# Kernel optimization log

Measured on AMD Instinct MI355X. Metric: run time of the kernel, lower is better.

## Reference

```python
import jax, jax.numpy as jnp
import numpy as np

GRAPH_SIZE = 128
ROWS = 3
COLS = 3
BATCH = 4096


def setup_inputs() -> dict:
    key = jax.random.key(0)
    k1, k2 = jax.random.split(key)
    x = jax.random.uniform(k1, (BATCH, GRAPH_SIZE, GRAPH_SIZE), dtype=jnp.float32)
    # kaiming_normal_ on a [rows, cols] 2D tensor: fan_in = cols, std = sqrt(2/fan_in)
    coef = jax.random.normal(k2, (ROWS, COLS), dtype=jnp.float32) * np.float32(np.sqrt(2.0 / COLS))
    return {"x": x, "coef": coef}


def reference(x, coef):
    # Faithful vectorized form of FACoef.forward.
    # Original per-sample math:
    #   a_series[0] = x@x ; a_series[i+1] = x @ a_series[i]   (a_series[i] = x^(i+2))
    #   term[i, j] = trace(ones @ a_series[i])**(j+1) / numel(x)**(i+j+2)
    # and trace(ones @ A) == sum of all entries of A.
    rows, cols = coef.shape
    G = x.shape[-1]
    x = x.reshape(-1, G, G)  # [B, G, G]
    n = jnp.float32(G * G)   # numel per graph

    p0 = jnp.matmul(x, x)    # x^2, [B, G, G]

    def step(p, _):
        s = p.sum(axis=(1, 2))          # trace(1 @ p) == sum(p), [B]
        return jnp.matmul(x, p), s      # next power x^(k+1)

    _, s = jax.lax.scan(step, p0, None, length=rows)  # s: [rows, B], s[i] = sum(x^(i+2))

    i = jnp.arange(rows, dtype=jnp.float32)[:, None, None]  # [rows,1,1]
    j = jnp.arange(cols, dtype=jnp.float32)[None, None, :]  # [1,1,cols]
    # terms: [rows, B, cols]
    terms = s[:, :, None] ** (j + 1.0) / n ** (i + j + 2.0)
    # per-sample scalar: sum(coef * terms.view(rows, cols))
    return jnp.sum(coef[:, None, :] * terms, axis=(0, 2))  # [B]
```

## Files before the change

kernel.cpp:

```cpp
#include <hip/hip_runtime.h>


#define G 128

typedef float v4f __attribute__((ext_vector_type(4)));

__global__ __launch_bounds__(512, 4) void facoef_kernel(
    const float* __restrict__ x, const float* __restrict__ coef,
    float* __restrict__ out) {
  const int b = blockIdx.x;
  const int tid = threadIdx.x;
  const int cg = tid & 31;
  const int rh = tid >> 5;

  __shared__ float part[16][128];
  __shared__ float u[128];
  __shared__ float Sp[3][2];

  const float* xb = x + (size_t)b * (G * G);

  v4f xs[8];
#pragma unroll
  for (int r = 0; r < 8; ++r) {
    xs[r] = *(const v4f*)(xb + (rh * 8 + r) * G + cg * 4);
  }

  v4f acc = xs[0];
#pragma unroll
  for (int r = 1; r < 8; ++r) acc += xs[r];
  *(v4f*)&part[rh][cg * 4] = acc;
  __syncthreads();

  if (tid < 128) {
    float s = 0.f;
#pragma unroll
    for (int h = 0; h < 16; ++h) s += part[h][tid];
    u[tid] = s;
  }
  __syncthreads();

  for (int k = 0; k < 3; ++k) {
    v4f a = {0.f, 0.f, 0.f, 0.f};
#pragma unroll
    for (int r = 0; r < 8; ++r) {
      float uv = u[rh * 8 + r];
      a += uv * xs[r];
    }
    *(v4f*)&part[rh][cg * 4] = a;
    __syncthreads();

    if (tid < 128) {
      float s = 0.f;
#pragma unroll
      for (int h = 0; h < 16; ++h) s += part[h][tid];
      float t = s;
#pragma unroll
      for (int off = 32; off > 0; off >>= 1) t += __shfl_xor(t, off, 64);
      if ((tid & 63) == 0) Sp[k][tid >> 6] = t;
      if (k < 2) u[tid] = s;
    }
    __syncthreads();
  }

  if (tid == 0) {
    double S[3];
#pragma unroll
    for (int k = 0; k < 3; ++k) S[k] = (double)Sp[k][0] + (double)Sp[k][1];
    const double n = (double)(G * G);
    double np[7];
    np[2] = n * n;
    np[3] = np[2] * n;
    np[4] = np[3] * n;
    np[5] = np[4] * n;
    np[6] = np[5] * n;
    double o = 0.0;
#pragma unroll
    for (int i = 0; i < 3; ++i) {
      double s1 = S[i], s2 = s1 * s1, s3 = s2 * s1;
      double sp[3] = {s1, s2, s3};
#pragma unroll
      for (int j = 0; j < 3; ++j) {
        o += (double)coef[i * 3 + j] * sp[j] / np[i + j + 2];
      }
    }
    out[b] = (float)o;
  }
}

extern "C" void kernel_launch(void* const* d_in, const int* in_sizes, int n_in,
                              void* d_out, int out_size, void* d_ws, size_t ws_size,
                              hipStream_t stream) {
  const float* x = (const float*)d_in[0];
  const float* coef = (const float*)d_in[1];
  float* out = (float*)d_out;
  const int batch = in_sizes[0] / (G * G);
  facoef_kernel<<<batch, 512, 0, stream>>>(x, coef, out);
}
```

Baseline: 45.79 us.

## Compute power sums via left/right vector products to cut sequential passes

Instead of three sequential passes of u<-u^T x, the kernel computes the column-sum vector u1 and the row-sum vector v1 = x·1 in the first pass. It then forms u2 = u1^T x and v2 = x v1 in one pass and gets sum(x^2), sum(x^3) and sum(x^4) as dot products u1·v1, u2·v1 and u2·v2. This removes one full pass over the register tile and several block barriers, at the cost of extra shuffle reductions. The occupancy hint is also raised to 8 blocks per CU.

New measurement: 47.36 us. 3.4% more time.

```diff
diff --git a/kernel.cpp b/kernel.cpp
--- a/kernel.cpp
+++ b/kernel.cpp
@@ -5,62 +5,95 @@
 
 typedef float v4f __attribute__((ext_vector_type(4)));
 
-__global__ __launch_bounds__(512, 4) void facoef_kernel(
+__global__ __launch_bounds__(512, 8) void facoef_kernel(
     const float* __restrict__ x, const float* __restrict__ coef,
     float* __restrict__ out) {
   const int b = blockIdx.x;
   const int tid = threadIdx.x;
   const int cg = tid & 31;
   const int rh = tid >> 5;
+  const int lane = tid & 63;
 
   __shared__ float part[16][128];
-  __shared__ float u[128];
+  __shared__ float u1s[128], v1s[128], v2s[128];
   __shared__ float Sp[3][2];
 
   const float* xb = x + (size_t)b * (G * G);
 
   v4f xs[8];
 #pragma unroll
-  for (int r = 0; r < 8; ++r) {
+  for (int r = 0; r < 8; ++r)
     xs[r] = *(const v4f*)(xb + (rh * 8 + r) * G + cg * 4);
-  }
 
   v4f acc = xs[0];
 #pragma unroll
   for (int r = 1; r < 8; ++r) acc += xs[r];
   *(v4f*)&part[rh][cg * 4] = acc;
+
+  float rs[8];
+#pragma unroll
+  for (int r = 0; r < 8; ++r) rs[r] = xs[r].x + xs[r].y + xs[r].z + xs[r].w;
+#pragma unroll
+  for (int off = 1; off < 32; off <<= 1) {
+#pragma unroll
+    for (int r = 0; r < 8; ++r) rs[r] += __shfl_xor(rs[r], off, 64);
+  }
+  if (cg == 0) {
+#pragma unroll
+    for (int r = 0; r < 8; ++r) v1s[rh * 8 + r] = rs[r];
+  }
   __syncthreads();
 
   if (tid < 128) {
     float s = 0.f;
 #pragma unroll
     for (int h = 0; h < 16; ++h) s += part[h][tid];
-    u[tid] = s;
+    u1s[tid] = s;
   }
   __syncthreads();
 
-  for (int k = 0; k < 3; ++k) {
-    v4f a = {0.f, 0.f, 0.f, 0.f};
+  v4f a = {0.f, 0.f, 0.f, 0.f};
+  const v4f v1f = *(const v4f*)&v1s[cg * 4];
+  float pd[8];
 #pragma unroll
-    for (int r = 0; r < 8; ++r) {
-      float uv = u[rh * 8 + r];
-      a += uv * xs[r];
+  for (int r = 0; r < 8; ++r) {
+    a += u1s[rh * 8 + r] * xs[r];
+    v4f p = xs[r] * v1f;
+    pd[r] = p.x + p.y + p.z + p.w;
+  }
+  *(v4f*)&part[rh][cg * 4] = a;
+#pragma unroll
+  for (int off = 1; off < 32; off <<= 1) {
+#pragma unroll
+    for (int r = 0; r < 8; ++r) pd[r] += __shfl_xor(pd[r], off, 64);
+  }
+  if (cg == 0) {
+#pragma unroll
+    for (int r = 0; r < 8; ++r) v2s[rh * 8 + r] = pd[r];
+  }
+  __syncthreads();
+
+  if (tid < 128) {
+    float u2 = 0.f;
+#pragma unroll
+    for (int h = 0; h < 16; ++h) u2 += part[h][tid];
+    const float u1v = u1s[tid], v1v = v1s[tid], v2v = v2s[tid];
+    float d2 = u1v * v1v;
+    float d3 = u2 * v1v;
+    float d4 = u2 * v2v;
+#pragma unroll
+    for (int off = 32; off > 0; off >>= 1) {
+      d2 += __shfl_xor(d2, off, 64);
+      d3 += __shfl_xor(d3, off, 64);
+      d4 += __shfl_xor(d4, off, 64);
     }
-    *(v4f*)&part[rh][cg * 4] = a;
-    __syncthreads();
-
-    if (tid < 128) {
-      float s = 0.f;
-#pragma unroll
-      for (int h = 0; h < 16; ++h) s += part[h][tid];
-      float t = s;
-#pragma unroll
-      for (int off = 32; off > 0; off >>= 1) t += __shfl_xor(t, off, 64);
-      if ((tid & 63) == 0) Sp[k][tid >> 6] = t;
-      if (k < 2) u[tid] = s;
+    if (lane == 0) {
+      Sp[0][tid >> 6] = d2;
+      Sp[1][tid >> 6] = d3;
+      Sp[2][tid >> 6] = d4;
     }
-    __syncthreads();
   }
+  __syncthreads();
 
   if (tid == 0) {
     double S[3];
```
